# Performance work log

Measured on AMD Instinct MI355X. Metric: run time of the kernel, lower is better.

## Reference

```python
import jax, jax.numpy as jnp
import numpy as np

THRESHOLD = 1.0


def setup_inputs() -> dict:
    key = jax.random.key(0)
    k1, k2 = jax.random.split(key)
    x = jax.random.normal(k1, (65536, 512), dtype=jnp.float32)
    label = jax.random.randint(k2, (65536,), 0, 1000, dtype=jnp.int64)
    return {"x": x, "label": label}


def reference(x, label):
    # Faithful vectorized translation of SiameseLoss.forward (including its quirks):
    #  - 'is_same' in the source is (same_identity == 0), i.e. True when labels DIFFER.
    #  - The margin branch squares only the second vector: norm(x1 - x2**2).
    half = x.shape[0] // 2
    x1 = x[:half]                       # [half, F]
    x2 = x[half:]                       # [half, F]
    labels_differ = label[:half] != label[half:]  # corresponds to source 'is_same'

    # Branch taken when labels differ: sum of squared differences per pair.
    d = x1 - x2
    loss_diff = jnp.sum(d * d, axis=1)  # [half]

    # Branch taken when labels match: relu(threshold - ||x1 - x2**2||_2).
    d2 = x1 - x2 * x2
    norm2 = jnp.sqrt(jnp.sum(d2 * d2, axis=1))  # [half]
    loss_same = jax.nn.relu(THRESHOLD - norm2)

    per_pair = jnp.where(labels_differ, loss_diff, loss_same)
    total = jnp.sum(per_pair) / (half * 2 * 2)
    return total.reshape(1)  # source returns a shape-[1] tensor
```

## Files before the change

kernel.cpp:

```cpp
#include <hip/hip_runtime.h>


constexpr int HALF    = 32768;
constexpr int D       = 512;
constexpr int NBLOCKS = 2048;
constexpr int THREADS = 256;
constexpr int WPB     = THREADS / 64;
constexpr int NWAVES  = NBLOCKS * WPB;
constexpr int PPW     = HALF / NWAVES;

__global__ __launch_bounds__(THREADS) void siamese_partial(
    const float* __restrict__ x, const int* __restrict__ label,
    float* __restrict__ partials) {
  const int lane  = threadIdx.x & 63;
  const int wave  = threadIdx.x >> 6;
  const int gwave = blockIdx.x * WPB + wave;

  float acc = 0.0f;
#pragma unroll
  for (int i = 0; i < PPW; ++i) {
    const int p = gwave + i * NWAVES;
    const float4* a = reinterpret_cast<const float4*>(x + (size_t)p * D);
    const float4* b = reinterpret_cast<const float4*>(x + (size_t)(HALF + p) * D);
    float4 a0 = a[lane];
    float4 a1 = a[lane + 64];
    float4 b0 = b[lane];
    float4 b1 = b[lane + 64];
    const int l1 = label[p];
    const int l2 = label[HALF + p];

    if (l1 != l2) {
      float dx = a0.x - b0.x, dy = a0.y - b0.y, dz = a0.z - b0.z, dw = a0.w - b0.w;
      acc = fmaf(dx, dx, acc); acc = fmaf(dy, dy, acc);
      acc = fmaf(dz, dz, acc); acc = fmaf(dw, dw, acc);
      dx = a1.x - b1.x; dy = a1.y - b1.y; dz = a1.z - b1.z; dw = a1.w - b1.w;
      acc = fmaf(dx, dx, acc); acc = fmaf(dy, dy, acc);
      acc = fmaf(dz, dz, acc); acc = fmaf(dw, dw, acc);
    } else {
      float ex = fmaf(-b0.x, b0.x, a0.x);
      float ey = fmaf(-b0.y, b0.y, a0.y);
      float ez = fmaf(-b0.z, b0.z, a0.z);
      float ew = fmaf(-b0.w, b0.w, a0.w);
      float sd2 = ex * ex;
      sd2 = fmaf(ey, ey, sd2); sd2 = fmaf(ez, ez, sd2); sd2 = fmaf(ew, ew, sd2);
      ex = fmaf(-b1.x, b1.x, a1.x);
      ey = fmaf(-b1.y, b1.y, a1.y);
      ez = fmaf(-b1.z, b1.z, a1.z);
      ew = fmaf(-b1.w, b1.w, a1.w);
      sd2 = fmaf(ex, ex, sd2); sd2 = fmaf(ey, ey, sd2);
      sd2 = fmaf(ez, ez, sd2); sd2 = fmaf(ew, ew, sd2);
#pragma unroll
      for (int m = 32; m >= 1; m >>= 1) sd2 += __shfl_xor(sd2, m);
      if (lane == 0) acc += fmaxf(0.0f, 1.0f - sqrtf(sd2));
    }
  }

#pragma unroll
  for (int m = 32; m >= 1; m >>= 1) acc += __shfl_xor(acc, m);

  __shared__ float lds[WPB];
  if (lane == 0) lds[wave] = acc;
  __syncthreads();
  if (threadIdx.x == 0) {
    float s = 0.0f;
#pragma unroll
    for (int w = 0; w < WPB; ++w) s += lds[w];
    partials[blockIdx.x] = s;
  }
}

__global__ __launch_bounds__(256) void siamese_reduce(
    const float* __restrict__ partials, float* __restrict__ out) {
  float s = 0.0f;
  for (int i = threadIdx.x; i < NBLOCKS; i += 256) s += partials[i];
#pragma unroll
  for (int m = 32; m >= 1; m >>= 1) s += __shfl_xor(s, m);
  __shared__ float lds[4];
  if ((threadIdx.x & 63) == 0) lds[threadIdx.x >> 6] = s;
  __syncthreads();
  if (threadIdx.x == 0) {
    float t = lds[0] + lds[1] + lds[2] + lds[3];
    out[0] = t * (1.0f / (float)(HALF * 4));
  }
}

extern "C" void kernel_launch(void* const* d_in, const int* in_sizes, int n_in,
                              void* d_out, int out_size, void* d_ws, size_t ws_size,
                              hipStream_t stream) {
  const float* x     = (const float*)d_in[0];
  const int*   label = (const int*)d_in[1];
  float* out      = (float*)d_out;
  float* partials = (float*)d_ws;

  siamese_partial<<<NBLOCKS, THREADS, 0, stream>>>(x, label, partials);
  siamese_reduce<<<1, 256, 0, stream>>>(partials, out);
}
```

Baseline: 28.51 us.

## Fuse final reduction into main kernel via fixed-point 64-bit atomic ticket counter

Removes the second reduce kernel. Each block converts its partial sum to fixed point and adds it to a single 64-bit counter whose upper bits count finished blocks. The block that brings the count to NBLOCKS writes the normalized result. This saves one kernel launch and the partials round trip, but adds a memset before the kernel, a contended atomic, and fixed-point quantization that assumes the total sum fits in 52 bits.

After: 44.96 us. +57.7%, slower.

```diff
diff --git a/kernel.cpp b/kernel.cpp
--- a/kernel.cpp
+++ b/kernel.cpp
@@ -9,9 +9,13 @@
 constexpr int NWAVES  = NBLOCKS * WPB;
 constexpr int PPW     = HALF / NWAVES;
 
-__global__ __launch_bounds__(THREADS) void siamese_partial(
+constexpr double            SCALE    = 262144.0;
+constexpr unsigned long long TICKET  = 1ULL << 52;
+constexpr unsigned long long SUMMASK = TICKET - 1ULL;
+
+__global__ __launch_bounds__(THREADS) void siamese_fused(
     const float* __restrict__ x, const int* __restrict__ label,
-    float* __restrict__ partials) {
+    unsigned long long* __restrict__ acc64, float* __restrict__ out) {
   const int lane  = threadIdx.x & 63;
   const int wave  = threadIdx.x >> 6;
   const int gwave = blockIdx.x * WPB + wave;
@@ -61,26 +65,18 @@
   __shared__ float lds[WPB];
   if (lane == 0) lds[wave] = acc;
   __syncthreads();
+
   if (threadIdx.x == 0) {
-    float s = 0.0f;
-#pragma unroll
-    for (int w = 0; w < WPB; ++w) s += lds[w];
-    partials[blockIdx.x] = s;
-  }
-}
-
-__global__ __launch_bounds__(256) void siamese_reduce(
-    const float* __restrict__ partials, float* __restrict__ out) {
-  float s = 0.0f;
-  for (int i = threadIdx.x; i < NBLOCKS; i += 256) s += partials[i];
-#pragma unroll
-  for (int m = 32; m >= 1; m >>= 1) s += __shfl_xor(s, m);
-  __shared__ float lds[4];
-  if ((threadIdx.x & 63) == 0) lds[threadIdx.x >> 6] = s;
-  __syncthreads();
-  if (threadIdx.x == 0) {
-    float t = lds[0] + lds[1] + lds[2] + lds[3];
-    out[0] = t * (1.0f / (float)(HALF * 4));
+    float s = lds[0] + lds[1] + lds[2] + lds[3];
+    unsigned long long u =
+        (unsigned long long)llrint((double)s * SCALE);
+    unsigned long long add  = TICKET + u;
+    unsigned long long old  = atomicAdd(acc64, add);
+    unsigned long long now  = old + add;
+    if ((now >> 52) == (unsigned long long)NBLOCKS) {
+      double total = (double)(now & SUMMASK) * (1.0 / SCALE);
+      out[0] = (float)(total / (double)(HALF * 4));
+    }
   }
 }
 
@@ -89,9 +85,9 @@
                               hipStream_t stream) {
   const float* x     = (const float*)d_in[0];
   const int*   label = (const int*)d_in[1];
-  float* out      = (float*)d_out;
-  float* partials = (float*)d_ws;
+  float* out = (float*)d_out;
+  unsigned long long* acc64 = (unsigned long long*)d_ws;
 
-  siamese_partial<<<NBLOCKS, THREADS, 0, stream>>>(x, label, partials);
-  siamese_reduce<<<1, 256, 0, stream>>>(partials, out);
+  hipMemsetAsync(d_ws, 0, 8, stream);
+  siamese_fused<<<NBLOCKS, THREADS, 0, stream>>>(x, label, acc64, out);
 }
```
